# Kernel tuning notes

Measured on AMD Instinct MI355X. Metric: run time of the kernel, lower is better.

The kernel has to match this reference:

```python
import jax, jax.numpy as jnp
import numpy as np
import math

# --- config (matches init_kwargs) ---
C = 128          # sphere_channels (multiplicity per l)
LMAX = 2
H = 8            # attention heads
B = 16           # graphs per batch (uniform)
M = 512          # nodes per graph
N = B * M        # 8192 nodes
E = 262144       # edges
D = C * sum(2 * l + 1 for l in range(LMAX + 1))  # 1152
_INV_SQRT_C = 1.0 / math.sqrt(C)


def irreps_linear(x, W):
    """e3nn o3.Linear irreps_node->irreps_node: per-l channel mixing, shared over m.
    x: [N, D], W: [LMAX+1, C, C]."""
    outs = []
    s = 0
    for l in range(LMAX + 1):
        d = 2 * l + 1
        blk = x[:, s:s + C * d].reshape(-1, C, d)          # [N, C, 2l+1]
        y = jnp.einsum('ncm,oc->nom', blk, W[l]) * _INV_SQRT_C
        outs.append(y.reshape(-1, C * d))
        s += C * d
    return jnp.concatenate(outs, axis=1)


def init_edge_rot_mat(edge_vec, edge_rand):
    """Faithful port of init_edge_rot_mat; edge_rand plays the role of rand_like."""
    dist = jnp.sqrt(jnp.sum(edge_vec ** 2, axis=1, keepdims=True))
    nx_ = edge_vec / dist
    e2 = edge_rand - 0.5
    e2 = e2 / jnp.sqrt(jnp.sum(e2 ** 2, axis=1, keepdims=True))
    e2b = jnp.stack([-e2[:, 1], e2[:, 0], e2[:, 2]], axis=1)
    e2c = jnp.stack([e2[:, 0], -e2[:, 2], e2[:, 1]], axis=1)
    dot = lambda a: jnp.abs(jnp.sum(a * nx_, axis=1, keepdims=True))
    vdb, vdc = dot(e2b), dot(e2c)
    e2 = jnp.where(dot(e2) > vdb, e2b, e2)
    e2 = jnp.where(dot(e2) > vdc, e2c, e2)
    nz = jnp.cross(nx_, e2)
    nz = nz / jnp.sqrt(jnp.sum(nz ** 2, axis=1, keepdims=True))
    ny = jnp.cross(nx_, nz)
    ny = ny / jnp.sqrt(jnp.sum(ny ** 2, axis=1, keepdims=True))
    rot_inv = jnp.stack([nz, nx_, -ny], axis=2)  # columns [z, x, -y]
    return jnp.transpose(rot_inv, (0, 2, 1))     # [E, 3, 3]


def setup_inputs() -> dict:
    key = jax.random.key(0)
    ks = jax.random.split(key, 10)
    node_features = jax.random.normal(ks[0], (N, D), dtype=jnp.float32)
    edge_vec = jax.random.normal(ks[1], (E, 3), dtype=jnp.float32)
    edge_rand = jax.random.uniform(ks[2], (E, 3), dtype=jnp.float32)
    edge_index = jax.random.randint(ks[3], (2, E), 0, N, dtype=jnp.int32)
    batch = jnp.repeat(jnp.arange(B, dtype=jnp.int32), M)
    W_q = jax.random.normal(ks[4], (LMAX + 1, C, C), dtype=jnp.float32)
    W_k = jax.random.normal(ks[5], (LMAX + 1, C, C), dtype=jnp.float32)
    W_v = jax.random.normal(ks[6], (LMAX + 1, C, C), dtype=jnp.float32)
    W_o = jax.random.normal(ks[7], (LMAX + 1, C, C), dtype=jnp.float32)
    gamma = jnp.ones((C,), dtype=jnp.float32)
    beta = jnp.zeros((C,), dtype=jnp.float32)
    return dict(node_features=node_features, edge_vec=edge_vec, edge_rand=edge_rand,
                W_q=W_q, W_k=W_k, W_v=W_v, W_o=W_o, gamma=gamma, beta=beta,
                edge_index=edge_index, batch=batch)


def reference(node_features, edge_vec, edge_rand, W_q, W_k, W_v, W_o, gamma, beta,
              edge_index, batch):
    # 1) per-edge rotation matrices (detached in the original)
    rot = jax.lax.stop_gradient(init_edge_rot_mat(edge_vec, edge_rand))

    x = node_features  # [N, D] equivariant irreps features

    # 2) SO2EquivariantGraphAttention: irreps q/k/v, dense per-graph multi-head attn
    q = irreps_linear(x, W_q)
    k = irreps_linear(x, W_k)
    v = irreps_linear(x, W_v)
    hd = D // H
    scale = 1.0 / math.sqrt(hd)
    # to_dense_batch with uniform graph sizes == reshape; mask all-true
    qd = q.reshape(B, M, H, hd).transpose(0, 2, 1, 3)  # [B,H,M,hd]
    kd = k.reshape(B, M, H, hd).transpose(0, 2, 1, 3)
    vd = v.reshape(B, M, H, hd).transpose(0, 2, 1, 3)
    scores = jnp.einsum('bhqd,bhkd->bhqk', qd, kd) * scale
    attn_w = jax.nn.softmax(scores, axis=-1)
    o = jnp.einsum('bhqk,bhkd->bhqd', attn_w, vd)
    o = o.transpose(0, 2, 1, 3).reshape(N, D)
    attn_out = irreps_linear(o, W_o)

    # residual connection
    x = x + attn_out

    # 3) EquivariantLayerNormV2: LayerNorm over l=0 dims only (first C)
    inv = x[:, :C]
    mu = jnp.mean(inv, axis=-1, keepdims=True)
    var = jnp.var(inv, axis=-1, keepdims=True)
    inv = (inv - mu) / jnp.sqrt(var + 1e-5) * gamma + beta

    # 4) S2Activation: SiLU on scalar (l=0) components, identity elsewhere
    inv = jax.nn.silu(inv)
    out = jnp.concatenate([inv, x[:, C:]], axis=1)
    return out, rot
```

## Files before the change

### kernel.cpp

```cpp
#include <hip/hip_runtime.h>
#include <hip/hip_bf16.h>

#define C_CH   128
#define DROW   1152
#define NNODE  8192
#define BATCH  16
#define MSEQ   512
#define NHEAD  8
#define HD     144
#define NEDGE  262144

typedef unsigned short ushort_t;
typedef __attribute__((ext_vector_type(8))) short bf16x8;
typedef __attribute__((ext_vector_type(4))) float f32x4;

__device__ __forceinline__ float ldf(const float* p) { return *p; }
__device__ __forceinline__ float ldf(const __hip_bfloat16* p) { return __bfloat162float(*p); }
__device__ __forceinline__ ushort_t f2bu(float x) {
    __hip_bfloat16 h = __float2bfloat16(x);
    return *reinterpret_cast<ushort_t*>(&h);
}
__device__ __forceinline__ float bu2f(ushort_t u) {
    return __bfloat162float(*reinterpret_cast<__hip_bfloat16*>(&u));
}
__device__ __forceinline__ unsigned u16of(const uint4 v, int ii) {
    const unsigned w = ((ii >> 1) == 0) ? v.x : ((ii >> 1) == 1) ? v.y :
                       ((ii >> 1) == 2) ? v.z : v.w;
    return (ii & 1) ? (w >> 16) : (w & 0xFFFFu);
}

#define KP2 136

template<int DL, int NPB>
__global__ __launch_bounds__(256) void lin_mfma_z(
    const float* __restrict__ X,
    const float* __restrict__ W0, const float* __restrict__ W1,
    const float* __restrict__ W2,
    __hip_bfloat16* __restrict__ Y0, __hip_bfloat16* __restrict__ Y1,
    __hip_bfloat16* __restrict__ Y2,
    int baseoff)
{
    constexpr int COLS = NPB * DL;
    constexpr int CT   = COLS / 16;
    __shared__ __align__(16) ushort_t Xs[COLS][KP2];
    __shared__ __align__(16) ushort_t Es[COLS][KP2];

    const int tid  = threadIdx.x;
    const int wave = tid >> 6;
    const int lane = tid & 63;
    const int l15  = lane & 15;
    const int quad = lane >> 4;
    const int n0   = blockIdx.x * NPB;
    const int z    = blockIdx.y;

    const float* W       = (z == 0) ? W0 : (z == 1 ? W1 : W2);
    __hip_bfloat16* Y    = (z == 0) ? Y0 : (z == 1 ? Y1 : Y2);

    for (int e4 = tid; e4 < NPB * 32 * DL; e4 += 256) {
        const int nb = e4 / (32 * DL);
        const int rr = (e4 - nb * (32 * DL)) * 4;
        const float4 xv = *reinterpret_cast<const float4*>(
            &X[(size_t)(n0 + nb) * DROW + baseoff + rr]);
        #pragma unroll
        for (int j = 0; j < 4; ++j) {
            const int r = rr + j, c = r / DL, m = r - c * DL;
            Xs[nb * DL + m][c] = f2bu(reinterpret_cast<const float*>(&xv)[j]);
        }
    }

    const float s = 0.08838834764831845f;

    bf16x8 aw[2][4];
    #pragma unroll
    for (int ot = 0; ot < 2; ++ot)
        #pragma unroll
        for (int kst = 0; kst < 4; ++kst) {
            const float* wp = &W[(size_t)(32 * wave + 16 * ot + l15) * 128 + kst * 32 + quad * 8];
            const float4 wa = *reinterpret_cast<const float4*>(wp);
            const float4 wb = *reinterpret_cast<const float4*>(wp + 4);
            ushort_t t[8] = {f2bu(wa.x), f2bu(wa.y), f2bu(wa.z), f2bu(wa.w),
                             f2bu(wb.x), f2bu(wb.y), f2bu(wb.z), f2bu(wb.w)};
            aw[ot][kst] = *reinterpret_cast<const bf16x8*>(t);
        }

    __syncthreads();

    f32x4 acc[CT][2];
    #pragma unroll
    for (int ct = 0; ct < CT; ++ct) {
        acc[ct][0] = (f32x4){0.f, 0.f, 0.f, 0.f};
        acc[ct][1] = (f32x4){0.f, 0.f, 0.f, 0.f};
    }
    #pragma unroll
    for (int kst = 0; kst < 4; ++kst)
        #pragma unroll
        for (int ct = 0; ct < CT; ++ct) {
            const bf16x8 b = *reinterpret_cast<const bf16x8*>(
                &Xs[ct * 16 + l15][kst * 32 + quad * 8]);
            acc[ct][0] = __builtin_amdgcn_mfma_f32_16x16x32_bf16(aw[0][kst], b, acc[ct][0], 0, 0, 0);
            acc[ct][1] = __builtin_amdgcn_mfma_f32_16x16x32_bf16(aw[1][kst], b, acc[ct][1], 0, 0, 0);
        }

    #pragma unroll
    for (int ct = 0; ct < CT; ++ct)
        #pragma unroll
        for (int ot = 0; ot < 2; ++ot) {
            ushort_t t[4] = {f2bu(acc[ct][ot][0] * s), f2bu(acc[ct][ot][1] * s),
                             f2bu(acc[ct][ot][2] * s), f2bu(acc[ct][ot][3] * s)};
            *reinterpret_cast<uint2*>(&Es[ct * 16 + l15][32 * wave + 16 * ot + quad * 4]) =
                *reinterpret_cast<const uint2*>(t);
        }
    __syncthreads();

    for (int e8 = tid; e8 < COLS * 16; e8 += 256) {
        const int nb = e8 / (16 * DL);
        const int r0 = (e8 - nb * (16 * DL)) * 8;
        const size_t ga = (size_t)(n0 + nb) * DROW + baseoff + r0;
        ushort_t t[8];
        #pragma unroll
        for (int j = 0; j < 8; ++j) {
            const int r = r0 + j;
            t[j] = Es[nb * DL + r % DL][r / DL];
        }
        *reinterpret_cast<uint4*>(&Y[ga]) = *reinterpret_cast<const uint4*>(t);
    }
}

template<int DL, int NPB, int NZ, int FUSE_LN, typename TX, typename TY>
__global__ __launch_bounds__(256) void lin_mfma(
    const TX* __restrict__ X,
    const float* __restrict__ W0, const float* __restrict__ W1,
    const float* __restrict__ W2,
    TY* __restrict__ Y0, TY* __restrict__ Y1, TY* __restrict__ Y2,
    const float* __restrict__ resid,
    const float* __restrict__ gamma, const float* __restrict__ beta,
    int baseoff)
{
    constexpr int COLS = NPB * DL;
    constexpr int CT   = COLS / 16;
    __shared__ __align__(16) ushort_t Xs[COLS][KP2];
    __shared__ __align__(16) ushort_t Es[COLS][KP2];

    const int tid  = threadIdx.x;
    const int wave = tid >> 6;
    const int lane = tid & 63;
    const int l15  = lane & 15;
    const int quad = lane >> 4;
    const int n0   = blockIdx.x * NPB;

    if constexpr (sizeof(TX) == 4) {
        for (int e4 = tid; e4 < NPB * 32 * DL; e4 += 256) {
            const int nb = e4 / (32 * DL);
            const int rr = (e4 - nb * (32 * DL)) * 4;
            const float4 xv = *reinterpret_cast<const float4*>(
                &X[(size_t)(n0 + nb) * DROW + baseoff + rr]);
            #pragma unroll
            for (int j = 0; j < 4; ++j) {
                const int r = rr + j, c = r / DL, m = r - c * DL;
                Xs[nb * DL + m][c] = f2bu(reinterpret_cast<const float*>(&xv)[j]);
            }
        }
    } else {
        for (int e8 = tid; e8 < NPB * 16 * DL; e8 += 256) {
            const int nb = e8 / (16 * DL);
            const int rr = (e8 - nb * (16 * DL)) * 8;
            const uint4 xv = *reinterpret_cast<const uint4*>(
                &X[(size_t)(n0 + nb) * DROW + baseoff + rr]);
            const ushort_t* xs = reinterpret_cast<const ushort_t*>(&xv);
            #pragma unroll
            for (int j = 0; j < 8; ++j) {
                const int r = rr + j, c = r / DL, m = r - c * DL;
                Xs[nb * DL + m][c] = xs[j];
            }
        }
    }

    const float s = 0.08838834764831845f;

    for (int z = 0; z < NZ; ++z) {
        const float* W = (z == 0) ? W0 : (z == 1 ? W1 : W2);
        TY* Y          = (z == 0) ? Y0 : (z == 1 ? Y1 : Y2);

        bf16x8 aw[2][4];
        #pragma unroll
        for (int ot = 0; ot < 2; ++ot)
            #pragma unroll
            for (int kst = 0; kst < 4; ++kst) {
                const float* wp = &W[(size_t)(32 * wave + 16 * ot + l15) * 128 + kst * 32 + quad * 8];
                const float4 wa = *reinterpret_cast<const float4*>(wp);
                const float4 wb = *reinterpret_cast<const float4*>(wp + 4);
                ushort_t t[8] = {f2bu(wa.x), f2bu(wa.y), f2bu(wa.z), f2bu(wa.w),
                                 f2bu(wb.x), f2bu(wb.y), f2bu(wb.z), f2bu(wb.w)};
                aw[ot][kst] = *reinterpret_cast<const bf16x8*>(t);
            }

        __syncthreads();

        f32x4 acc[CT][2];
        #pragma unroll
        for (int ct = 0; ct < CT; ++ct) {
            acc[ct][0] = (f32x4){0.f, 0.f, 0.f, 0.f};
            acc[ct][1] = (f32x4){0.f, 0.f, 0.f, 0.f};
        }
        #pragma unroll
        for (int kst = 0; kst < 4; ++kst)
            #pragma unroll
            for (int ct = 0; ct < CT; ++ct) {
                const bf16x8 b = *reinterpret_cast<const bf16x8*>(
                    &Xs[ct * 16 + l15][kst * 32 + quad * 8]);
                acc[ct][0] = __builtin_amdgcn_mfma_f32_16x16x32_bf16(aw[0][kst], b, acc[ct][0], 0, 0, 0);
                acc[ct][1] = __builtin_amdgcn_mfma_f32_16x16x32_bf16(aw[1][kst], b, acc[ct][1], 0, 0, 0);
            }

        #pragma unroll
        for (int ct = 0; ct < CT; ++ct)
            #pragma unroll
            for (int ot = 0; ot < 2; ++ot) {
                ushort_t t[4] = {f2bu(acc[ct][ot][0] * s), f2bu(acc[ct][ot][1] * s),
                                 f2bu(acc[ct][ot][2] * s), f2bu(acc[ct][ot][3] * s)};
                *reinterpret_cast<uint2*>(&Es[ct * 16 + l15][32 * wave + 16 * ot + quad * 4]) =
                    *reinterpret_cast<const uint2*>(t);
            }
        __syncthreads();

        if constexpr (FUSE_LN) {
            const int nb = tid >> 2, cc = tid & 3;
            float y[32];
            const float* xr = resid + (size_t)(n0 + nb) * DROW + cc * 32;
            float s1 = 0.f, s2 = 0.f;
            #pragma unroll
            for (int j4 = 0; j4 < 8; ++j4) {
                const float4 rv = *reinterpret_cast<const float4*>(xr + j4 * 4);
                #pragma unroll
                for (int j = 0; j < 4; ++j) {
                    const float v = bu2f(Es[nb][cc * 32 + j4 * 4 + j]) +
                                    reinterpret_cast<const float*>(&rv)[j];
                    y[j4 * 4 + j] = v; s1 += v; s2 += v * v;
                }
            }
            s1 += __shfl_xor(s1, 1); s2 += __shfl_xor(s2, 1);
            s1 += __shfl_xor(s1, 2); s2 += __shfl_xor(s2, 2);
            const float mean = s1 * (1.0f / 128.0f);
            const float var  = s2 * (1.0f / 128.0f) - mean * mean;
            const float rstd = rsqrtf(var + 1e-5f);
            float* op = (float*)Y + (size_t)(n0 + nb) * DROW + cc * 32;
            #pragma unroll
            for (int j4 = 0; j4 < 8; ++j4) {
                float4 ov;
                #pragma unroll
                for (int j = 0; j < 4; ++j) {
                    const int c = cc * 32 + j4 * 4 + j;
                    float t = (y[j4 * 4 + j] - mean) * rstd * gamma[c] + beta[c];
                    reinterpret_cast<float*>(&ov)[j] = t / (1.0f + __expf(-t));
                }
                *reinterpret_cast<float4*>(op + j4 * 4) = ov;
            }
        } else {
            for (int e8 = tid; e8 < COLS * 16; e8 += 256) {
                const int nb = e8 / (16 * DL);
                const int r0 = (e8 - nb * (16 * DL)) * 8;
                const size_t ga = (size_t)(n0 + nb) * DROW + baseoff + r0;
                if constexpr (sizeof(TY) == 2) {
                    ushort_t t[8];
                    #pragma unroll
                    for (int j = 0; j < 8; ++j) {
                        const int r = r0 + j;
                        t[j] = Es[nb * DL + r % DL][r / DL];
                    }
                    *reinterpret_cast<uint4*>(&Y[ga]) = *reinterpret_cast<const uint4*>(t);
                } else {
                    #pragma unroll
                    for (int j4 = 0; j4 < 2; ++j4) {
                        const float4 rv = *reinterpret_cast<const float4*>(&resid[ga + j4 * 4]);
                        float4 ov;
                        #pragma unroll
                        for (int j = 0; j < 4; ++j) {
                            const int r = r0 + j4 * 4 + j;
                            reinterpret_cast<float*>(&ov)[j] =
                                bu2f(Es[nb * DL + r % DL][r / DL]) +
                                reinterpret_cast<const float*>(&rv)[j];
                        }
                        *reinterpret_cast<float4*>(&((float*)Y)[ga + j4 * 4]) = ov;
                    }
                }
            }
        }
    }
}

#define KPAD  168
#define VROWS 160
#define VPAD2 72
#define PPAD  68

__global__ __launch_bounds__(256, 2) void attn_kernel(
    const __hip_bfloat16* __restrict__ Q, const __hip_bfloat16* __restrict__ K,
    const __hip_bfloat16* __restrict__ V, __hip_bfloat16* __restrict__ O)
{
    __shared__ __align__(16) ushort_t ksqs[64][KPAD];
    __shared__ __align__(16) ushort_t vst[VROWS][VPAD2];
    __shared__ __align__(16) ushort_t ps[128][PPAD];

    const int tid  = threadIdx.x;
    const int wave = tid >> 6;
    const int lane = tid & 63;
    const int l15  = lane & 15;
    const int quad = lane >> 4;

    const int bid = blockIdx.x;
    const int xcd = bid & 7;
    const int j   = bid >> 3;
    const int bh  = xcd * 16 + (j >> 2);
    const int q0  = (j & 3) * 128;
    const int h   = bh & 7;
    const int b   = bh >> 3;
    const size_t rowbase = (size_t)b * MSEQ * DROW + (size_t)h * HD;
    const float EXSCALE = 0.12022458674074695f;

    const int r0 = tid / 18,          g0 = tid % 18;
    const int r1 = (tid + 256) / 18,  g1 = (tid + 256) % 18;
    const int r2 = (tid + 512) / 18,  g2 = (tid + 512) % 18;
    const int r3 = (tid + 768) / 18,  g3 = (tid + 768) % 18;
    const int r4 = (tid + 1024) / 18, g4 = (tid + 1024) % 18;
    const int ko0 = r0 * DROW + g0 * 8, ko1 = r1 * DROW + g1 * 8;
    const int ko2 = r2 * DROW + g2 * 8, ko3 = r3 * DROW + g3 * 8;
    const int ko4 = r4 * DROW + g4 * 8;
    ushort_t* kld0 = &ksqs[r0][g0 * 8];
    ushort_t* kld1 = &ksqs[r1][g1 * 8];
    ushort_t* kld2 = &ksqs[r2][g2 * 8];
    ushort_t* kld3 = &ksqs[r3][g3 * 8];
    ushort_t* kld4 = &ksqs[r4][g4 * 8];
    const int rqa = tid / 18,          ga = tid % 18;
    const int rqb = (tid + 256) / 18,  gb = (tid + 256) % 18;
    const int voa = (rqa * 4) * DROW + ga * 8;
    const int vob = (rqb * 4) * DROW + gb * 8;
    const bool hasK4 = (tid < 128);
    const bool hasVB = (tid < 32);

    uint4 kp0, kp1, kp2, kp3, kp4;
    uint4 va0, va1, va2, va3, vb0, vb1, vb2, vb3;

#define LOAD_K(KC) do { \
        const __hip_bfloat16* kb_ = K + rowbase + (size_t)((KC) * 64) * DROW; \
        kp0 = *reinterpret_cast<const uint4*>(kb_ + ko0); \
        kp1 = *reinterpret_cast<const uint4*>(kb_ + ko1); \
        kp2 = *reinterpret_cast<const uint4*>(kb_ + ko2); \
        kp3 = *reinterpret_cast<const uint4*>(kb_ + ko3); \
        if (hasK4) kp4 = *reinterpret_cast<const uint4*>(kb_ + ko4); \
    } while (0)

#define LOAD_V(KC) do { \
        const __hip_bfloat16* vbp_ = V + rowbase + (size_t)((KC) * 64) * DROW; \
        va0 = *reinterpret_cast<const uint4*>(vbp_ + voa); \
        va1 = *reinterpret_cast<const uint4*>(vbp_ + voa + DROW); \
        va2 = *reinterpret_cast<const uint4*>(vbp_ + voa + 2 * DROW); \
        va3 = *reinterpret_cast<const uint4*>(vbp_ + voa + 3 * DROW); \
        if (hasVB) { \
            vb0 = *reinterpret_cast<const uint4*>(vbp_ + vob); \
            vb1 = *reinterpret_cast<const uint4*>(vbp_ + vob + DROW); \
            vb2 = *reinterpret_cast<const uint4*>(vbp_ + vob + 2 * DROW); \
            vb3 = *reinterpret_cast<const uint4*>(vbp_ + vob + 3 * DROW); \
        } \
    } while (0)

#define WRITE_KV() do { \
        *reinterpret_cast<uint4*>(kld0) = kp0; \
        *reinterpret_cast<uint4*>(kld1) = kp1; \
        *reinterpret_cast<uint4*>(kld2) = kp2; \
        *reinterpret_cast<uint4*>(kld3) = kp3; \
        if (hasK4) *reinterpret_cast<uint4*>(kld4) = kp4; \
        _Pragma("unroll") \
        for (int ii = 0; ii < 8; ++ii) { \
            uint2 pk; \
            pk.x = u16of(va0, ii) | (u16of(va1, ii) << 16); \
            pk.y = u16of(va2, ii) | (u16of(va3, ii) << 16); \
            *reinterpret_cast<uint2*>(&vst[ga * 8 + ii][rqa * 4]) = pk; \
        } \
        if (hasVB) { \
            _Pragma("unroll") \
            for (int ii = 0; ii < 8; ++ii) { \
                uint2 pk; \
                pk.x = u16of(vb0, ii) | (u16of(vb1, ii) << 16); \
                pk.y = u16of(vb2, ii) | (u16of(vb3, ii) << 16); \
                *reinterpret_cast<uint2*>(&vst[gb * 8 + ii][rqb * 4]) = pk; \
            } \
        } \
    } while (0)

    LOAD_K(0);
    LOAD_V(0);

    for (int idx = tid; idx < 64 * 16; idx += 256)
        ksqs[idx >> 4][HD + (idx & 15)] = 0;
    for (int idx = tid; idx < 16 * VPAD2; idx += 256)
        vst[144 + idx / VPAD2][idx % VPAD2] = (idx / VPAD2 == 0) ? (ushort_t)0x3F80 : (ushort_t)0;

    bf16x8 aq[2][5];
    for (int hh = 0; hh < 2; ++hh) {
        __syncthreads();
        for (int idx = tid; idx < 64 * 18; idx += 256) {
            const int r = idx / 18, g = idx % 18;
            *reinterpret_cast<uint4*>(&ksqs[r][g * 8]) =
                *reinterpret_cast<const uint4*>(&Q[rowbase + (size_t)(q0 + hh * 64 + r) * DROW + g * 8]);
        }
        __syncthreads();
        if ((wave >> 1) == hh) {
            #pragma unroll
            for (int rt = 0; rt < 2; ++rt)
                #pragma unroll
                for (int kst = 0; kst < 5; ++kst)
                    aq[rt][kst] = *reinterpret_cast<const bf16x8*>(
                        &ksqs[32 * (wave & 1) + rt * 16 + l15][kst * 32 + quad * 8]);
        }
    }

    f32x4 oacc[2][10];
    #pragma unroll
    for (int rt = 0; rt < 2; ++rt)
        #pragma unroll
        for (int nt = 0; nt < 10; ++nt) oacc[rt][nt] = (f32x4){0.f, 0.f, 0.f, 0.f};

    for (int kc = 0; kc < 8; ++kc) {
        __syncthreads();
        WRITE_KV();
        __syncthreads();
        if (kc < 7) LOAD_K(kc + 1);

        f32x4 sc[2][4];
        #pragma unroll
        for (int rt = 0; rt < 2; ++rt)
            #pragma unroll
            for (int kt = 0; kt < 4; ++kt) sc[rt][kt] = (f32x4){0.f, 0.f, 0.f, 0.f};
        #pragma unroll
        for (int kst = 0; kst < 5; ++kst) {
            bf16x8 bk[4];
            #pragma unroll
            for (int kt = 0; kt < 4; ++kt)
                bk[kt] = *reinterpret_cast<const bf16x8*>(
                    &ksqs[kt * 16 + l15][kst * 32 + quad * 8]);
            #pragma unroll
            for (int rt = 0; rt < 2; ++rt)
                #pragma unroll
                for (int kt = 0; kt < 4; ++kt)
                    sc[rt][kt] = __builtin_amdgcn_mfma_f32_16x16x32_bf16(aq[rt][kst], bk[kt], sc[rt][kt], 0, 0, 0);
        }

        if (kc < 7) LOAD_V(kc + 1);

        #pragma unroll
        for (int rt = 0; rt < 2; ++rt)
            #pragma unroll
            for (int kt = 0; kt < 4; ++kt)
                #pragma unroll
                for (int i = 0; i < 4; ++i)
                    ps[32 * wave + 16 * rt + quad * 4 + i][16 * kt + l15] =
                        f2bu(exp2f(sc[rt][kt][i] * EXSCALE));

        #pragma unroll
        for (int kp = 0; kp < 2; ++kp) {
            bf16x8 pa[2];
            #pragma unroll
            for (int rt = 0; rt < 2; ++rt)
                pa[rt] = *reinterpret_cast<const bf16x8*>(
                    &ps[32 * wave + 16 * rt + l15][kp * 32 + quad * 8]);
            #pragma unroll
            for (int nt = 0; nt < 10; ++nt) {
                const bf16x8 bv = *reinterpret_cast<const bf16x8*>(
                    &vst[nt * 16 + l15][kp * 32 + quad * 8]);
                #pragma unroll
                for (int rt = 0; rt < 2; ++rt)
                    oacc[rt][nt] = __builtin_amdgcn_mfma_f32_16x16x32_bf16(pa[rt], bv, oacc[rt][nt], 0, 0, 0);
            }
        }
    }

    #pragma unroll
    for (int rt = 0; rt < 2; ++rt) {
        #pragma unroll
        for (int i = 0; i < 4; ++i) {
            const float l = __shfl(oacc[rt][9][i], lane & 48);
            const float inv = 1.0f / l;
            const int row = q0 + 32 * wave + 16 * rt + quad * 4 + i;
            const size_t rb = rowbase + (size_t)row * DROW;
            #pragma unroll
            for (int nt = 0; nt < 9; ++nt)
                O[rb + nt * 16 + l15] = __float2bfloat16(oacc[rt][nt][i] * inv);
        }
    }
#undef LOAD_K
#undef LOAD_V
#undef WRITE_KV
}

__global__ __launch_bounds__(256) void rot_kernel(
    const float* __restrict__ ev, const float* __restrict__ er,
    float* __restrict__ rot)
{
    const int e = blockIdx.x * 256 + threadIdx.x;
    if (e >= NEDGE) return;
    const float vx = ev[e * 3 + 0], vy = ev[e * 3 + 1], vz = ev[e * 3 + 2];
    const float d = sqrtf(vx * vx + vy * vy + vz * vz);
    const float nx0 = vx / d, nx1 = vy / d, nx2 = vz / d;
    float r0 = er[e * 3 + 0] - 0.5f;
    float r1 = er[e * 3 + 1] - 0.5f;
    float r2 = er[e * 3 + 2] - 0.5f;
    const float rn = sqrtf(r0 * r0 + r1 * r1 + r2 * r2);
    r0 /= rn; r1 /= rn; r2 /= rn;
    const float b0 = -r1, b1 = r0, b2v = r2;
    const float c0 = r0, c1 = -r2, c2 = r1;
    const float vd0 = fabsf(r0 * nx0 + r1 * nx1 + r2 * nx2);
    const float vdb = fabsf(b0 * nx0 + b1 * nx1 + b2v * nx2);
    const float vdc = fabsf(c0 * nx0 + c1 * nx1 + c2 * nx2);
    if (vd0 > vdb) { r0 = b0; r1 = b1; r2 = b2v; }
    const float vd1 = fabsf(r0 * nx0 + r1 * nx1 + r2 * nx2);
    if (vd1 > vdc) { r0 = c0; r1 = c1; r2 = c2; }
    float z0 = nx1 * r2 - nx2 * r1;
    float z1 = nx2 * r0 - nx0 * r2;
    float z2 = nx0 * r1 - nx1 * r0;
    const float zn = sqrtf(z0 * z0 + z1 * z1 + z2 * z2);
    z0 /= zn; z1 /= zn; z2 /= zn;
    float y0 = nx1 * z2 - nx2 * z1;
    float y1 = nx2 * z0 - nx0 * z2;
    float y2 = nx0 * z1 - nx1 * z0;
    const float yn = sqrtf(y0 * y0 + y1 * y1 + y2 * y2);
    y0 /= yn; y1 /= yn; y2 /= yn;
    float* rp = rot + (size_t)e * 9;
    rp[0] = z0;   rp[1] = z1;   rp[2] = z2;
    rp[3] = nx0;  rp[4] = nx1;  rp[5] = nx2;
    rp[6] = -y0;  rp[7] = -y1;  rp[8] = -y2;
}

extern "C" void kernel_launch(void* const* d_in, const int* in_sizes, int n_in,
                              void* d_out, int out_size, void* d_ws, size_t ws_size,
                              hipStream_t stream)
{
    (void)in_sizes; (void)n_in; (void)out_size; (void)ws_size;
    const float* x     = (const float*)d_in[0];
    const float* ev    = (const float*)d_in[1];
    const float* er    = (const float*)d_in[2];
    const float* Wq    = (const float*)d_in[3];
    const float* Wk    = (const float*)d_in[4];
    const float* Wv    = (const float*)d_in[5];
    const float* Wo    = (const float*)d_in[6];
    const float* gamma = (const float*)d_in[7];
    const float* beta  = (const float*)d_in[8];

    float* out = (float*)d_out;
    float* rot = out + (size_t)NNODE * DROW;

    const size_t ND = (size_t)NNODE * DROW;
    __hip_bfloat16* q = (__hip_bfloat16*)d_ws;
    __hip_bfloat16* k = q + ND;
    __hip_bfloat16* v = k + ND;
    __hip_bfloat16* o = v + ND;

    rot_kernel<<<NEDGE / 256, 256, 0, stream>>>(ev, er, rot);

    lin_mfma_z<1, 64><<<dim3(NNODE / 64, 3), 256, 0, stream>>>(
        x, Wq, Wk, Wv, q, k, v, 0);
    lin_mfma_z<3, 32><<<dim3(NNODE / 32, 3), 256, 0, stream>>>(
        x, Wq + 16384, Wk + 16384, Wv + 16384, q, k, v, 128);
    lin_mfma_z<5, 16><<<dim3(NNODE / 16, 3), 256, 0, stream>>>(
        x, Wq + 32768, Wk + 32768, Wv + 32768, q, k, v, 512);

    attn_kernel<<<(MSEQ / 128) * NHEAD * BATCH, 256, 0, stream>>>(q, k, v, o);

    lin_mfma<1, 64, 1, 1, __hip_bfloat16, float><<<NNODE / 64, 256, 0, stream>>>(
        o, Wo, nullptr, nullptr, out, nullptr, nullptr, x, gamma, beta, 0);
    lin_mfma<3, 32, 1, 0, __hip_bfloat16, float><<<NNODE / 32, 256, 0, stream>>>(
        o, Wo + 16384, nullptr, nullptr, out, nullptr, nullptr, x, nullptr, nullptr, 128);
    lin_mfma<5, 16, 1, 0, __hip_bfloat16, float><<<NNODE / 16, 256, 0, stream>>>(
        o, Wo + 32768, nullptr, nullptr, out, nullptr, nullptr, x, nullptr, nullptr, 512);
}
```

Before: 240.6 us.

## Fuse Q/K/V projections for all l-blocks into one kernel

Replaces three per-l launches, each split three ways over Q/K/V, with a single kernel. Each block loads 16 full node rows into shared memory once and loops over Q, K and V, applying all three per-l weight blocks. This stops x from being read nine times and removes launch overhead. The cost is fewer blocks (512) with a serial z loop, more syncs, and weights re-read from global memory per block.

New measurement: 251.1 us. +4.4%, slower.

```diff
diff --git a/kernel.cpp b/kernel.cpp
--- a/kernel.cpp
+++ b/kernel.cpp
@@ -31,98 +31,113 @@
 
 #define KP2 136
 
-template<int DL, int NPB>
-__global__ __launch_bounds__(256) void lin_mfma_z(
+__global__ __launch_bounds__(256) void qkv_fused(
     const float* __restrict__ X,
-    const float* __restrict__ W0, const float* __restrict__ W1,
-    const float* __restrict__ W2,
-    __hip_bfloat16* __restrict__ Y0, __hip_bfloat16* __restrict__ Y1,
-    __hip_bfloat16* __restrict__ Y2,
-    int baseoff)
+    const float* __restrict__ Wq, const float* __restrict__ Wk,
+    const float* __restrict__ Wv,
+    __hip_bfloat16* __restrict__ Yq, __hip_bfloat16* __restrict__ Yk,
+    __hip_bfloat16* __restrict__ Yv)
 {
-    constexpr int COLS = NPB * DL;
-    constexpr int CT   = COLS / 16;
-    __shared__ __align__(16) ushort_t Xs[COLS][KP2];
-    __shared__ __align__(16) ushort_t Es[COLS][KP2];
+    __shared__ __align__(16) ushort_t Xs[144][KP2];
+    __shared__ __align__(16) ushort_t Es[144][KP2];
 
     const int tid  = threadIdx.x;
     const int wave = tid >> 6;
     const int lane = tid & 63;
     const int l15  = lane & 15;
     const int quad = lane >> 4;
-    const int n0   = blockIdx.x * NPB;
-    const int z    = blockIdx.y;
-
-    const float* W       = (z == 0) ? W0 : (z == 1 ? W1 : W2);
-    __hip_bfloat16* Y    = (z == 0) ? Y0 : (z == 1 ? Y1 : Y2);
-
-    for (int e4 = tid; e4 < NPB * 32 * DL; e4 += 256) {
-        const int nb = e4 / (32 * DL);
-        const int rr = (e4 - nb * (32 * DL)) * 4;
+    const int n0   = blockIdx.x * 16;
+
+    for (int e4 = tid; e4 < 16 * 288; e4 += 256) {
+        const int nb = e4 / 288;
+        const int rr = (e4 - nb * 288) * 4;
         const float4 xv = *reinterpret_cast<const float4*>(
-            &X[(size_t)(n0 + nb) * DROW + baseoff + rr]);
+            &X[(size_t)(n0 + nb) * DROW + rr]);
         #pragma unroll
         for (int j = 0; j < 4; ++j) {
-            const int r = rr + j, c = r / DL, m = r - c * DL;
-            Xs[nb * DL + m][c] = f2bu(reinterpret_cast<const float*>(&xv)[j]);
+            const int r = rr + j;
+            int col, c;
+            if (r < 128)      { col = nb; c = r; }
+            else if (r < 512) { const int t = r - 128; c = t / 3; col = 16 + nb * 3 + (t - c * 3); }
+            else              { const int t = r - 512; c = t / 5; col = 64 + nb * 5 + (t - c * 5); }
+            Xs[col][c] = f2bu(reinterpret_cast<const float*>(&xv)[j]);
         }
     }
 
     const float s = 0.08838834764831845f;
 
-    bf16x8 aw[2][4];
-    #pragma unroll
-    for (int ot = 0; ot < 2; ++ot)
-        #pragma unroll
-        for (int kst = 0; kst < 4; ++kst) {
-            const float* wp = &W[(size_t)(32 * wave + 16 * ot + l15) * 128 + kst * 32 + quad * 8];
-            const float4 wa = *reinterpret_cast<const float4*>(wp);
-            const float4 wb = *reinterpret_cast<const float4*>(wp + 4);
-            ushort_t t[8] = {f2bu(wa.x), f2bu(wa.y), f2bu(wa.z), f2bu(wa.w),
-                             f2bu(wb.x), f2bu(wb.y), f2bu(wb.z), f2bu(wb.w)};
-            aw[ot][kst] = *reinterpret_cast<const bf16x8*>(t);
-        }
-
     __syncthreads();
 
-    f32x4 acc[CT][2];
-    #pragma unroll
-    for (int ct = 0; ct < CT; ++ct) {
-        acc[ct][0] = (f32x4){0.f, 0.f, 0.f, 0.f};
-        acc[ct][1] = (f32x4){0.f, 0.f, 0.f, 0.f};
-    }
-    #pragma unroll
-    for (int kst = 0; kst < 4; ++kst)
-        #pragma unroll
-        for (int ct = 0; ct < CT; ++ct) {
-            const bf16x8 b = *reinterpret_cast<const bf16x8*>(
-                &Xs[ct * 16 + l15][kst * 32 + quad * 8]);
-            acc[ct][0] = __builtin_amdgcn_mfma_f32_16x16x32_bf16(aw[0][kst], b, acc[ct][0], 0, 0, 0);
-            acc[ct][1] = __builtin_amdgcn_mfma_f32_16x16x32_bf16(aw[1][kst], b, acc[ct][1], 0, 0, 0);
-        }
-
-    #pragma unroll
-    for (int ct = 0; ct < CT; ++ct)
-        #pragma unroll
-        for (int ot = 0; ot < 2; ++ot) {
-            ushort_t t[4] = {f2bu(acc[ct][ot][0] * s), f2bu(acc[ct][ot][1] * s),
-                             f2bu(acc[ct][ot][2] * s), f2bu(acc[ct][ot][3] * s)};
-            *reinterpret_cast<uint2*>(&Es[ct * 16 + l15][32 * wave + 16 * ot + quad * 4]) =
-                *reinterpret_cast<const uint2*>(t);
-        }
-    __syncthreads();
-
-    for (int e8 = tid; e8 < COLS * 16; e8 += 256) {
-        const int nb = e8 / (16 * DL);
-        const int r0 = (e8 - nb * (16 * DL)) * 8;
-        const size_t ga = (size_t)(n0 + nb) * DROW + baseoff + r0;
-        ushort_t t[8];
-        #pragma unroll
-        for (int j = 0; j < 8; ++j) {
-            const int r = r0 + j;
-            t[j] = Es[nb * DL + r % DL][r / DL];
-        }
-        *reinterpret_cast<uint4*>(&Y[ga]) = *reinterpret_cast<const uint4*>(t);
+    for (int z = 0; z < 3; ++z) {
+        const float* Wz        = (z == 0) ? Wq : (z == 1 ? Wk : Wv);
+        __hip_bfloat16* Y      = (z == 0) ? Yq : (z == 1 ? Yk : Yv);
+
+        f32x4 acc[9][2];
+        #pragma unroll
+        for (int ct = 0; ct < 9; ++ct) {
+            acc[ct][0] = (f32x4){0.f, 0.f, 0.f, 0.f};
+            acc[ct][1] = (f32x4){0.f, 0.f, 0.f, 0.f};
+        }
+
+        #pragma unroll
+        for (int lg = 0; lg < 3; ++lg) {
+            const int woff   = lg * 16384;
+            const int ctlo   = (lg == 0) ? 0 : (lg == 1 ? 1 : 4);
+            const int cthi   = (lg == 0) ? 1 : (lg == 1 ? 4 : 9);
+            const float* W   = Wz + woff;
+
+            bf16x8 aw[2][4];
+            #pragma unroll
+            for (int ot = 0; ot < 2; ++ot)
+                #pragma unroll
+                for (int kst = 0; kst < 4; ++kst) {
+                    const float* wp = &W[(size_t)(32 * wave + 16 * ot + l15) * 128 + kst * 32 + quad * 8];
+                    const float4 wa = *reinterpret_cast<const float4*>(wp);
+                    const float4 wb = *reinterpret_cast<const float4*>(wp + 4);
+                    ushort_t t[8] = {f2bu(wa.x), f2bu(wa.y), f2bu(wa.z), f2bu(wa.w),
+                                     f2bu(wb.x), f2bu(wb.y), f2bu(wb.z), f2bu(wb.w)};
+                    aw[ot][kst] = *reinterpret_cast<const bf16x8*>(t);
+                }
+
+            #pragma unroll
+            for (int kst = 0; kst < 4; ++kst)
+                #pragma unroll 9
+                for (int ct = ctlo; ct < cthi; ++ct) {
+                    const bf16x8 b = *reinterpret_cast<const bf16x8*>(
+                        &Xs[ct * 16 + l15][kst * 32 + quad * 8]);
+                    acc[ct][0] = __builtin_amdgcn_mfma_f32_16x16x32_bf16(aw[0][kst], b, acc[ct][0], 0, 0, 0);
+                    acc[ct][1] = __builtin_amdgcn_mfma_f32_16x16x32_bf16(aw[1][kst], b, acc[ct][1], 0, 0, 0);
+                }
+        }
+
+        #pragma unroll
+        for (int ct = 0; ct < 9; ++ct)
+            #pragma unroll
+            for (int ot = 0; ot < 2; ++ot) {
+                ushort_t t[4] = {f2bu(acc[ct][ot][0] * s), f2bu(acc[ct][ot][1] * s),
+                                 f2bu(acc[ct][ot][2] * s), f2bu(acc[ct][ot][3] * s)};
+                *reinterpret_cast<uint2*>(&Es[ct * 16 + l15][32 * wave + 16 * ot + quad * 4]) =
+                    *reinterpret_cast<const uint2*>(t);
+            }
+        __syncthreads();
+
+        for (int e8 = tid; e8 < 16 * 144; e8 += 256) {
+            const int nb = e8 / 144;
+            const int rr = (e8 - nb * 144) * 8;
+            ushort_t t[8];
+            #pragma unroll
+            for (int j = 0; j < 8; ++j) {
+                const int r = rr + j;
+                int col, o;
+                if (r < 128)      { col = nb; o = r; }
+                else if (r < 512) { const int u = r - 128; o = u / 3; col = 16 + nb * 3 + (u - o * 3); }
+                else              { const int u = r - 512; o = u / 5; col = 64 + nb * 5 + (u - o * 5); }
+                t[j] = Es[col][o];
+            }
+            *reinterpret_cast<uint4*>(&Y[(size_t)(n0 + nb) * DROW + rr]) =
+                *reinterpret_cast<const uint4*>(t);
+        }
+        __syncthreads();
     }
 }
 
@@ -556,12 +571,7 @@
 
     rot_kernel<<<NEDGE / 256, 256, 0, stream>>>(ev, er, rot);
 
-    lin_mfma_z<1, 64><<<dim3(NNODE / 64, 3), 256, 0, stream>>>(
-        x, Wq, Wk, Wv, q, k, v, 0);
-    lin_mfma_z<3, 32><<<dim3(NNODE / 32, 3), 256, 0, stream>>>(
-        x, Wq + 16384, Wk + 16384, Wv + 16384, q, k, v, 128);
-    lin_mfma_z<5, 16><<<dim3(NNODE / 16, 3), 256, 0, stream>>>(
-        x, Wq + 32768, Wk + 32768, Wv + 32768, q, k, v, 512);
+    qkv_fused<<<NNODE / 16, 256, 0, stream>>>(x, Wq, Wk, Wv, q, k, v);
 
     attn_kernel<<<(MSEQ / 128) * NHEAD * BATCH, 256, 0, stream>>>(q, k, v, o);
 
```
